# Kernel optimization log

Hardware: AMD Instinct MI355X
Metric: run time of the kernel (lower is better)

The kernel has to match this reference:

```python
import jax, jax.numpy as jnp
import numpy as np
from jax import lax

B, S, T = 32, 400, 100
V, OOV = 32000, 100
E, U, AU, GP, ENC = 512, 256, 256, 256, 512


def setup_inputs() -> dict:
    key = jax.random.key(0)
    ks = jax.random.split(key, 24)
    r = lambda k, shp: 0.02 * jax.random.normal(k, shp, dtype=jnp.float32)
    inp = {
        "gt_tokens": jax.random.randint(ks[0], (B, T), 0, V, dtype=jnp.int32),
        "extended_input_tokens": jax.random.randint(ks[1], (B, S), 0, V + OOV, dtype=jnp.int32),
        "enc_output": jax.random.normal(ks[2], (B, S, ENC), dtype=jnp.float32),
        "enc_attn": jax.random.normal(ks[3], (B, S, AU), dtype=jnp.float32),
        "h0": jnp.zeros((B, U), jnp.float32),
        "c0": jnp.zeros((B, U), jnp.float32),
        # learned parameters
        "emb": r(ks[4], (V, E)),
        "lstm_kernel": r(ks[5], (E, 4 * U)),
        "lstm_rec": r(ks[6], (U, 4 * U)),
        "lstm_bias": jnp.zeros((4 * U,), jnp.float32),
        "attn_Wd": r(ks[7], (2 * U, AU)),
        "attn_bd": jnp.zeros((AU,), jnp.float32),
        "attn_Wc": r(ks[8], (1, AU)),
        "attn_Wa": r(ks[9], (AU, 1)),
        "clf_W1": r(ks[10], (U, U)),
        "clf_b1": jnp.zeros((U,), jnp.float32),
        "clf_W2": r(ks[11], (U, V)),
        "clf_b2": jnp.zeros((V,), jnp.float32),
        "gp_Ws": r(ks[12], (2 * U, GP)),
        "gp_Wc": r(ks[13], (ENC, GP)),
        "gp_Wi": r(ks[14], (E, GP)),
        "gp_bi": jnp.zeros((GP,), jnp.float32),
        "gp_Wg": r(ks[15], (GP, 1)),
    }
    return inp


def _decode(gt_tokens, extended_input_tokens, enc_output, enc_attn, h0, c0,
            emb, lstm_kernel, lstm_rec, lstm_bias, attn_Wd, attn_bd, attn_Wc,
            attn_Wa, clf_W1, clf_b1, clf_W2, clf_b2, gp_Ws, gp_Wc, gp_Wi,
            gp_bi, gp_Wg):
    Bn, Sn = extended_input_tokens.shape
    gt_vec = emb[gt_tokens]                      # [B,T,E] teacher-forced inputs
    xs = jnp.swapaxes(gt_vec, 0, 1)              # [T,B,E]
    batch_idx = jnp.arange(Bn)[:, None]

    def step(carry, x):
        h, c, cov = carry                        # [B,U],[B,U],[B,S]
        # single-step LSTM (TF gate order i,f,g,o)
        z = x @ lstm_kernel + h @ lstm_rec + lstm_bias
        i_, f_, g_, o_ = jnp.split(z, 4, axis=-1)
        c = jax.nn.sigmoid(f_) * c + jax.nn.sigmoid(i_) * jnp.tanh(g_)
        h = jax.nn.sigmoid(o_) * jnp.tanh(c)
        dec_state = jnp.concatenate([h, c], axis=1)          # [B,2U]
        # Bahdanau attention with coverage
        dec_attn = dec_state @ attn_Wd + attn_bd             # [B,AU]
        cov_attn = cov[:, :, None] * attn_Wc[0]              # [B,S,AU]
        scores = jnp.tanh(enc_attn + cov_attn + dec_attn[:, None, :]) @ attn_Wa
        a = jax.nn.softmax(scores, axis=1)[:, :, 0]          # [B,S]
        c_vec = jnp.einsum('bse,bs->be', enc_output, a)      # [B,ENC]
        cov_loss = jnp.sum(jnp.minimum(cov, a), axis=1)      # [B]
        cov = cov + a
        # pg: faithful scalar quirk ([0,0,0] of broadcast sum in original)
        g = dec_state[0] @ gp_Ws + c_vec[0] @ gp_Wc + (x[0] @ gp_Wi + gp_bi)
        pg = jax.nn.sigmoid((g @ gp_Wg)[0])
        # vocab distribution, extended with OOV zeros
        vocab_p = jax.nn.softmax((h @ clf_W1 + clf_b1) @ clf_W2 + clf_b2, axis=-1)
        vocab_p = jnp.concatenate([vocab_p, jnp.zeros((Bn, OOV), vocab_p.dtype)], axis=1)
        # copy distribution via scatter-add of attention onto extended ids
        sent_p = jnp.zeros((Bn, V + OOV), a.dtype).at[batch_idx, extended_input_tokens].add(a)
        final = pg * vocab_p + (1.0 - pg) * sent_p           # [B,V+OOV]
        tok = jnp.argmax(final, axis=1).astype(jnp.int32)
        return (h, c, cov), (final, tok, cov_loss)

    cov0 = jnp.zeros((Bn, Sn), jnp.float32)
    _, (probs, seqs, cov_losses) = lax.scan(step, (h0, c0, cov0), xs)
    return (jnp.swapaxes(probs, 0, 1),       # [B,T,V+OOV]
            jnp.swapaxes(seqs, 0, 1),        # [B,T]
            jnp.swapaxes(cov_losses, 0, 1))  # [B,T]


def reference(gt_tokens, extended_input_tokens, enc_output, enc_attn, h0, c0,
              emb, lstm_kernel, lstm_rec, lstm_bias, attn_Wd, attn_bd,
              attn_Wc, attn_Wa, clf_W1, clf_b1, clf_W2, clf_b2, gp_Ws, gp_Wc,
              gp_Wi, gp_bi, gp_Wg):
    return _decode(gt_tokens, extended_input_tokens, enc_output, enc_attn, h0,
                   c0, emb, lstm_kernel, lstm_rec, lstm_bias, attn_Wd,
                   attn_bd, attn_Wc, attn_Wa, clf_W1, clf_b1, clf_W2, clf_b2,
                   gp_Ws, gp_Wc, gp_Wi, gp_bi, gp_Wg)
```

## Files before the change

### kernel.cpp

```cpp
#include <hip/hip_runtime.h>
#include <hip/hip_bf16.h>

#define Bn 32
#define Sn 400
#define Tn 100
#define Vn 32000
#define OOVn 100
#define VEn 32100
#define En 512
#define Un 256
#define AUn 256
#define GPn 256
#define ENCn 512
#define Z4n 1024
#define NPB 250

typedef __attribute__((ext_vector_type(8))) short bf16x8;
typedef __attribute__((ext_vector_type(4))) float f32x4;
typedef unsigned short ushort_t;
typedef unsigned long long u64;

__device__ __forceinline__ float rcp_f(float x){ return __builtin_amdgcn_rcpf(x); }
__device__ __forceinline__ float tanh_fast(float x){
  float e2 = __expf(2.f*x);
  return 1.f - 2.f*rcp_f(e2 + 1.f);
}
__device__ __forceinline__ float sigmoid_f(float x){ return 1.f/(1.f+__expf(-x)); }
__device__ __forceinline__ ushort_t f2bf(float f){
  unsigned u = __float_as_uint(f);
  unsigned r = (u + 0x7FFFu + ((u>>16)&1u)) >> 16;
  return (ushort_t)r;
}
__device__ __forceinline__ u64 shfl_xor_u64(u64 v, int m){
  unsigned lo = (unsigned)v, hi = (unsigned)(v>>32);
  lo = (unsigned)__shfl_xor((int)lo, m);
  hi = (unsigned)__shfl_xor((int)hi, m);
  return ((u64)hi<<32)|(u64)lo;
}

__device__ __forceinline__ void st_rlx(float* p, float v){
  __hip_atomic_store(p, v, __ATOMIC_RELAXED, __HIP_MEMORY_SCOPE_AGENT);
}
__device__ __forceinline__ float ld_rlx(const float* p){
  return __hip_atomic_load(p, __ATOMIC_RELAXED, __HIP_MEMORY_SCOPE_AGENT);
}
__device__ __forceinline__ void st_rlxu(unsigned* p, unsigned v){
  __hip_atomic_store(p, v, __ATOMIC_RELAXED, __HIP_MEMORY_SCOPE_AGENT);
}
__device__ __forceinline__ void st_rlx64(u64* p, u64 v){
  __hip_atomic_store(p, v, __ATOMIC_RELAXED, __HIP_MEMORY_SCOPE_AGENT);
}
__device__ __forceinline__ u64 ld_rlx64(const u64* p){
  return __hip_atomic_load(p, __ATOMIC_RELAXED, __HIP_MEMORY_SCOPE_AGENT);
}
__device__ __forceinline__ void st_flag(unsigned* p, unsigned v){
  __hip_atomic_store(p, v, __ATOMIC_RELAXED, __HIP_MEMORY_SCOPE_AGENT);
}
__device__ __forceinline__ unsigned ld_flag(const unsigned* p){
  return __hip_atomic_load(p, __ATOMIC_RELAXED, __HIP_MEMORY_SCOPE_AGENT);
}


__global__ __launch_bounds__(256) void k_zx(const int* __restrict__ gt,
    const float* __restrict__ emb, const float* __restrict__ Wk,
    const float* __restrict__ bias, float* __restrict__ Zx,
    const float* __restrict__ W2, ushort_t* __restrict__ W2T,
    unsigned* __restrict__ bars, unsigned* __restrict__ bars2,
    float* __restrict__ covloss){
  __shared__ __align__(16) char zbuf[16640];
  float (*As)[17] = (float(*)[17])zbuf;
  float (*Bs)[65] = (float(*)[65])(zbuf + 4352);
  int*   tok_lds  = (int*)(zbuf + 4352 + 4160);
  int r0 = blockIdx.x * 64;
  int c0 = blockIdx.y * 64;
  int tid = threadIdx.x;
  int ty = tid >> 4, tx16 = tid & 15;
  if (blockIdx.x == 0){
    int y = blockIdx.y;
    #pragma unroll
    for (int i = 0; i < 2; ++i){
      int idx = y*512 + i*256 + tid;
      bars[idx] = 0u;
      if (idx < NPB*32) bars2[idx] = 0u;
    }
    if (tid < 200) covloss[y*200 + tid] = 0.f;
  }
  if (tid < 64){
    int r = r0 + tid;
    tok_lds[tid] = gt[(r & 31)*Tn + (r >> 5)];
  }
  __syncthreads();
  float acc[4][4] = {};
  for (int k0 = 0; k0 < En; k0 += 16){
    #pragma unroll
    for (int p = 0; p < 4; ++p){
      int row = (tid>>4) + p*16, kk = tid & 15;
      As[row][kk] = emb[(size_t)tok_lds[row]*En + k0 + kk];
    }
    #pragma unroll
    for (int p = 0; p < 4; ++p){
      int kk = (tid>>6) + p*4, cc = tid & 63;
      Bs[kk][cc] = Wk[(size_t)(k0+kk)*Z4n + c0 + cc];
    }
    __syncthreads();
    #pragma unroll
    for (int kk = 0; kk < 16; ++kk){
      float av[4], bv[4];
      #pragma unroll
      for (int i=0;i<4;++i) av[i] = As[ty*4+i][kk];
      #pragma unroll
      for (int j=0;j<4;++j) bv[j] = Bs[kk][tx16*4+j];
      #pragma unroll
      for (int i=0;i<4;++i)
        #pragma unroll
        for (int j=0;j<4;++j) acc[i][j] += av[i]*bv[j];
    }
    __syncthreads();
  }
  #pragma unroll
  for (int i=0;i<4;++i){
    int row = r0 + ty*4 + i;
    #pragma unroll
    for (int j=0;j<4;++j){
      int col = c0 + tx16*4 + j;
      Zx[(size_t)row*Z4n + col] = acc[i][j] + bias[col];
    }
  }
  float (*tl)[65] = (float(*)[65])zbuf;
  int tx = tid & 63, ty4 = tid >> 6;
  int bid = blockIdx.x*16 + blockIdx.y;
  for (int rep = 0; rep < 3; ++rep){
    int tile = bid + rep*800;
    if (tile >= 2000) break;
    int n0 = (tile % 500) * 64, k0 = (tile / 500) * 64;
    __syncthreads();
    #pragma unroll
    for (int i = 0; i < 16; ++i){
      int kk = ty4 + i*4;
      tl[kk][tx] = W2[(size_t)(k0+kk)*Vn + n0 + tx];
    }
    __syncthreads();
    #pragma unroll
    for (int i = 0; i < 16; ++i){
      int n = ty4 + i*4;
      W2T[(size_t)(n0+n)*Un + k0 + tx] = f2bf(tl[tx][n]);
    }
  }
}


__global__ __launch_bounds__(1024, 1) void k_loop(
    const float* __restrict__ Zx, const float* __restrict__ Wr,
    const float* __restrict__ Wd, const float* __restrict__ bd,
    const float* __restrict__ Wc, const float* __restrict__ Wa,
    const float* __restrict__ enc_attn,
    const float* __restrict__ h0, const float* __restrict__ c0,
    float* __restrict__ h_all, float* __restrict__ decp,
    float* __restrict__ c0_all, float* __restrict__ a_all,
    float* __restrict__ covloss, float* __restrict__ spart,
    unsigned* __restrict__ bars){
  __shared__ float Wr_lds[256*128];
  __shared__ float hfull[Un];
  __shared__ float ppart[8][132];
  __shared__ float zx_lds[128];
  __shared__ float zfull[128];
  __shared__ float hnew[32], cown[32];
  __shared__ float dec_lds[AUn];
  __shared__ float cov_lds[50], sc_lds[50];
  __shared__ float wred[16];
  __shared__ float red8[8];

  const int b = blockIdx.x & 31, k = blockIdx.x >> 5;
  const int tid = threadIdx.x, lane = tid & 63, w = tid >> 6;
  unsigned* flags = bars + b*8*32;
  unsigned* myflag = flags + k*32;

  for (int idx = tid; idx < 256*128; idx += 1024){
    int u = idx >> 7, jl = idx & 127;
    int gcol = 32*k + (jl & 31) + 256*(jl >> 5);
    Wr_lds[idx] = Wr[(size_t)u*Z4n + gcol];
  }
  if (tid < 32) cown[tid] = c0[b*Un + 32*k + tid];
  if (tid < 50) cov_lds[tid] = 0.f;
  const float4 wc4 = *(const float4*)(Wc + lane*4);
  const float4 wa4 = *(const float4*)(Wa + lane*4);
  if (tid < 256) hfull[tid] = h0[b*Un + tid];
  if (tid >= 256 && tid < 384){
    int jl = tid - 256;
    int gcol = 32*k + (jl & 31) + 256*(jl >> 5);
    zx_lds[jl] = Zx[(size_t)(0*Bn + b)*Z4n + gcol];
  }
  __syncthreads();

  {
    int p = tid >> 7, jl = tid & 127;
    float acc = 0.f;
    const float* wr = Wr_lds + (p*32)*128 + jl;
    const float* hb = hfull + p*32;
    #pragma unroll 8
    for (int uu = 0; uu < 32; ++uu) acc += hb[uu]*wr[uu*128];
    ppart[p][jl] = acc;
  }
  __syncthreads();
  if (tid < 128){
    float s = zx_lds[tid];
    #pragma unroll
    for (int q = 0; q < 8; ++q) s += ppart[q][tid];
    zfull[tid] = s;
  }
  __syncthreads();
  if (tid < 32){
    float zi = zfull[tid], zf = zfull[32+tid], zg = zfull[64+tid], zo = zfull[96+tid];
    float cn = sigmoid_f(zf)*cown[tid] + sigmoid_f(zi)*tanhf(zg);
    float hn = sigmoid_f(zo)*tanhf(cn);
    cown[tid] = cn; hnew[tid] = hn;
    int col = 32*k + tid;
    st_rlx(h_all + (size_t)(0*Bn + b)*Un + col, hn);
    if (b == 0) c0_all[0*Un + col] = cn;
  }
  __syncthreads();
  if (tid < 256){
    int c = tid;
    float acc = 0.f;
    const float* wdh = Wd + (size_t)(32*k)*AUn + c;
    #pragma unroll 8
    for (int u = 0; u < 32; ++u) acc += hnew[u]*wdh[(size_t)u*AUn];
    const float* wdc = Wd + (size_t)(Un + 32*k)*AUn + c;
    #pragma unroll 8
    for (int u = 0; u < 32; ++u) acc += cown[u]*wdc[(size_t)u*AUn];
    st_rlx(decp + (size_t)(b*8 + k)*256 + c, acc);
  }
  __syncthreads();
  if (tid == 0) st_flag(myflag, 1u);

  for (int t = 0; t < Tn; ++t){
    const int cur = t & 1, oth = cur ^ 1;
    if (tid < 8){
      while (ld_flag(flags + tid*32) < (unsigned)(t+1))
        __builtin_amdgcn_s_sleep(1);
    }
    __syncthreads();
    if (tid < 256){
      hfull[tid] = ld_rlx(h_all + (size_t)(t*Bn + b)*Un + tid);
    } else if (tid < 512){
      int c = tid - 256;
      float s = bd[c];
      const float* dp = decp + (size_t)cur*(Bn*8*256) + (size_t)(b*8)*256 + c;
      #pragma unroll
      for (int q = 0; q < 8; ++q) s += ld_rlx(dp + q*256);
      dec_lds[c] = s;
    } else if (tid < 520){
      red8[tid-512] = (t > 0) ? ld_rlx(spart + oth*(Bn*8) + b*8 + (tid-512)) : 0.f;
    } else if (tid >= 576 && tid < 704 && t + 1 < Tn){
      int jl = tid - 576;
      int gcol = 32*k + (jl & 31) + 256*(jl >> 5);
      zx_lds[jl] = Zx[(size_t)((t+1)*Bn + b)*Z4n + gcol];
    }
    __syncthreads();
    if (t > 0 && w == 0){
      float pv = (lane < 8) ? red8[lane] : 0.f;
      pv += __shfl_xor(pv, 1); pv += __shfl_xor(pv, 2); pv += __shfl_xor(pv, 4);
      float inv = 1.f / __shfl(pv, 0);
      float clp = 0.f;
      if (lane < 50){
        float aa = sc_lds[lane] * inv;
        float co = cov_lds[lane];
        a_all[(size_t)((t-1)*Bn + b)*Sn + 50*k + lane] = aa;
        clp = fminf(co, aa);
        cov_lds[lane] = co + aa;
      }
      #pragma unroll
      for (int m = 1; m < 64; m <<= 1) clp += __shfl_xor(clp, m);
      if (lane == 0) atomicAdd(&covloss[b*Tn + (t-1)], clp);
    }
    {
      int p = tid >> 7, jl = tid & 127;
      float acc = 0.f;
      const float* wr = Wr_lds + (p*32)*128 + jl;
      const float* hb = hfull + p*32;
      #pragma unroll 8
      for (int uu = 0; uu < 32; ++uu) acc += hb[uu]*wr[uu*128];
      ppart[p][jl] = acc;
    }
    __syncthreads();
    if (tid < 128 && t + 1 < Tn){
      float s = zx_lds[tid];
      #pragma unroll
      for (int q = 0; q < 8; ++q) s += ppart[q][tid];
      zfull[tid] = s;
    }
    __syncthreads();
    if (tid < 32 && t + 1 < Tn){
      float zi = zfull[tid], zf = zfull[32+tid], zg = zfull[64+tid], zo = zfull[96+tid];
      float cn = sigmoid_f(zf)*cown[tid] + sigmoid_f(zi)*tanhf(zg);
      float hn = sigmoid_f(zo)*tanhf(cn);
      cown[tid] = cn; hnew[tid] = hn;
      int col = 32*k + tid;
      st_rlx(h_all + (size_t)((t+1)*Bn + b)*Un + col, hn);
      if (b == 0) c0_all[(t+1)*Un + col] = cn;
    }
    __syncthreads();
    if (w < 4){
      if (t + 1 < Tn){
        int c = tid;
        float acc = 0.f;
        const float* wdh = Wd + (size_t)(32*k)*AUn + c;
        #pragma unroll 8
        for (int u = 0; u < 32; ++u) acc += hnew[u]*wdh[(size_t)u*AUn];
        const float* wdc = Wd + (size_t)(Un + 32*k)*AUn + c;
        #pragma unroll 8
        for (int u = 0; u < 32; ++u) acc += cown[u]*wdc[(size_t)u*AUn];
        st_rlx(decp + (size_t)oth*(Bn*8*256) + (size_t)(b*8 + k)*256 + c, acc);
      }
    } else {
      const float4 da = *(const float4*)(dec_lds + lane*4);
      float wsum = 0.f;
      for (int sl = w - 4; sl < 50; sl += 12){
        float cvv = cov_lds[sl];
        const float4 e = *(const float4*)(enc_attn + ((size_t)(b*Sn + 50*k + sl))*AUn + lane*4);
        float psc = tanh_fast(e.x + cvv*wc4.x + da.x)*wa4.x
                  + tanh_fast(e.y + cvv*wc4.y + da.y)*wa4.y
                  + tanh_fast(e.z + cvv*wc4.z + da.z)*wa4.z
                  + tanh_fast(e.w + cvv*wc4.w + da.w)*wa4.w;
        #pragma unroll
        for (int m = 1; m < 64; m <<= 1) psc += __shfl_xor(psc, m);
        if (lane == 0){
          float ev = __expf(psc);
          sc_lds[sl] = ev;
          wsum += ev;
        }
      }
      if (lane == 0) wred[w] = wsum;
    }
    __syncthreads();
    if (tid == 0){
      float S = 0.f;
      #pragma unroll
      for (int q = 4; q < 16; ++q) S += wred[q];
      st_rlx(spart + cur*(Bn*8) + b*8 + k, S);
    }
    __syncthreads();
    if (tid == 0) st_flag(myflag, (unsigned)(t + 2));
  }

  if (tid < 8){
    while (ld_flag(flags + tid*32) < (unsigned)(Tn + 1))
      __builtin_amdgcn_s_sleep(1);
  }
  __syncthreads();
  if (tid < 8) red8[tid] = ld_rlx(spart + ((Tn-1)&1)*(Bn*8) + b*8 + tid);
  __syncthreads();
  if (w == 0){
    float pv = (lane < 8) ? red8[lane] : 0.f;
    pv += __shfl_xor(pv, 1); pv += __shfl_xor(pv, 2); pv += __shfl_xor(pv, 4);
    float inv = 1.f / __shfl(pv, 0);
    float clp = 0.f;
    if (lane < 50){
      float aa = sc_lds[lane] * inv;
      float co = cov_lds[lane];
      a_all[(size_t)((Tn-1)*Bn + b)*Sn + 50*k + lane] = aa;
      clp = fminf(co, aa);
    }
    #pragma unroll
    for (int m = 1; m < 64; m <<= 1) clp += __shfl_xor(clp, m);
    if (lane == 0) atomicAdd(&covloss[b*Tn + (Tn-1)], clp);
  }
}


__global__ __launch_bounds__(512, 1) void k_post(
    const float* __restrict__ h_all, const float* __restrict__ W1,
    const float* __restrict__ b1, ushort_t* __restrict__ hid,
    const int* __restrict__ gt, const float* __restrict__ emb,
    const float* __restrict__ gpWi, const float* __restrict__ gpbi,
    const float* __restrict__ a_all, const float* __restrict__ enc_out,
    const float* __restrict__ c0_all, const float* __restrict__ gpWs,
    const float* __restrict__ gpWc, const float* __restrict__ gpWg,
    float* __restrict__ pg, const ushort_t* __restrict__ W2T,
    const float* __restrict__ b2, float* __restrict__ Sp,
    float* __restrict__ Ssum, u64* __restrict__ Ap,
    float* __restrict__ probs, const int* __restrict__ ext,
    float* __restrict__ seqs, unsigned* __restrict__ bars2){
  __shared__ __align__(16) char sb[135168];
  __shared__ u64 wmax8[8];
  __shared__ float red4[4];
  const int gid = blockIdx.x, tid = threadIdx.x;
  const int lane = tid & 63, w = tid >> 6;
  unsigned* myflag = bars2 + gid*32;

  if (gid < 100){
    int t = gid;
    float* hl = (float*)sb;
    for (int i = tid; i < Bn*Un; i += 512) hl[i] = h_all[(size_t)t*Bn*Un + i];
    __syncthreads();
    int j = tid & 255, p = tid >> 8;
    float bj = b1[j];
    float acc[16];
    #pragma unroll
    for (int i = 0; i < 16; ++i) acc[i] = bj;
    for (int u = 0; u < Un; ++u){
      float wv = W1[u*Un + j];
      const float* hp = hl + (p*16)*Un + u;
      #pragma unroll
      for (int i = 0; i < 16; ++i) acc[i] += hp[i*Un] * wv;
    }
    __syncthreads();
    ushort_t* hidL = (ushort_t*)sb;
    #pragma unroll
    for (int i = 0; i < 16; ++i) hidL[(p*16+i)*Un + j] = f2bf(acc[i]);
    __syncthreads();
    unsigned* hw = (unsigned*)hid + (size_t)t*4096;
    const unsigned* hs = (const unsigned*)hidL;
    for (int i = tid; i < 4096; i += 512) st_rlxu(hw + i, hs[i]);
  } else if (gid < 200){
    int t = gid - 100;
    float* al = (float*)sb;
    float* cv = al + 400;
    float* xl = cv + 512;
    for (int s = tid; s < Sn; s += 512) al[s] = a_all[(size_t)(t*Bn)*Sn + s];
    for (int i = tid; i < En; i += 512) xl[i] = emb[(size_t)gt[t]*En + i];
    __syncthreads();
    if (tid < ENCn){
      float acc = 0.f;
      for (int s = 0; s < Sn; ++s) acc += enc_out[(size_t)s*ENCn + tid]*al[s];
      cv[tid] = acc;
    }
    __syncthreads();
    if (tid < 256){
      int j = tid;
      float g = gpbi[j];
      for (int u = 0; u < En; ++u) g += xl[u]*gpWi[u*GPn + j];
      const float* h0r = h_all + (size_t)t*Bn*Un;
      const float* c0r = c0_all + t*Un;
      for (int u = 0; u < Un; ++u) g += h0r[u]*gpWs[u*GPn + j];
      for (int u = 0; u < Un; ++u) g += c0r[u]*gpWs[(Un+u)*GPn + j];
      for (int e = 0; e < ENCn; ++e) g += cv[e]*gpWc[e*GPn + j];
      float v = g * gpWg[j];
      #pragma unroll
      for (int m = 1; m < 64; m <<= 1) v += __shfl_xor(v, m);
      if (lane == 0) red4[w] = v;
    }
    __syncthreads();
    if (tid == 0)
      st_rlx(&pg[t], 1.f/(1.f+__expf(-(red4[0]+red4[1]+red4[2]+red4[3]))));
  }
  __syncthreads();
  if (tid == 0) st_flag(myflag, 1u);
  if (tid < NPB){ while (ld_flag(bars2 + tid*32) < 1u) __builtin_amdgcn_s_sleep(1); }
  __syncthreads();

  ushort_t* Bs = (ushort_t*)sb;
  const int slice = gid % 125, gx = gid / 125;
  const int n0 = slice * 256;
  {
    int rr = tid >> 1, half = (tid & 1) * 128;
    const ushort_t* gb = W2T + (size_t)(n0 + rr)*Un + half;
    ushort_t* lb = Bs + rr*264 + half;
    #pragma unroll
    for (int j2 = 0; j2 < 16; ++j2)
      *((uint4*)lb + j2) = *((const uint4*)gb + j2);
  }
  __syncthreads();
  const int cbase = gx ? 13 : 0;
  const int nch   = gx ? 12 : 13;

  for (int ci = 0; ci < nch; ++ci){
    int r0 = (cbase + ci) * 128;
    bf16x8 af[8];
    {
      const ushort_t* ar = hid + (size_t)(r0 + w*16 + (lane&15))*Un + (lane>>4)*8;
      #pragma unroll
      for (int kk = 0; kk < 8; ++kk) af[kk] = *(const bf16x8*)(ar + kk*32);
    }
    f32x4 acc[16];
    #pragma unroll
    for (int i = 0; i < 16; ++i) acc[i] = (f32x4){0.f,0.f,0.f,0.f};
    #pragma unroll
    for (int kk = 0; kk < 8; ++kk){
      #pragma unroll
      for (int nt = 0; nt < 16; ++nt){
        bf16x8 bf = *(const bf16x8*)(Bs + (nt*16 + (lane&15))*264 + kk*32 + (lane>>4)*8);
        acc[nt] = __builtin_amdgcn_mfma_f32_16x16x32_bf16(af[kk], bf, acc[nt], 0, 0, 0);
      }
    }
    float rs[4] = {0.f,0.f,0.f,0.f};
    #pragma unroll
    for (int nt = 0; nt < 16; ++nt){
      int v = n0 + nt*16 + (lane&15);
      float b2v = b2[v];
      #pragma unroll
      for (int i = 0; i < 4; ++i) rs[i] += __expf(acc[nt][i] + b2v);
    }
    #pragma unroll
    for (int m = 1; m < 16; m <<= 1)
      #pragma unroll
      for (int i = 0; i < 4; ++i) rs[i] += __shfl_xor(rs[i], m);
    if ((lane&15) == 0){
      int rowloc = w*16 + (lane>>4)*4;
      #pragma unroll
      for (int i = 0; i < 4; ++i)
        st_rlx(&Sp[(size_t)slice*3200 + r0 + rowloc + i], rs[i]);
    }
  }
  __syncthreads();
  if (tid == 0) st_flag(myflag, 2u);
  if (tid < NPB){ while (ld_flag(bars2 + tid*32) < 2u) __builtin_amdgcn_s_sleep(1); }
  __syncthreads();

  if (gid < 7){
    int r = gid*512 + tid;
    if (r < 3200){
      float s = 0.f;
      for (int sl = 0; sl < 125; ++sl) s += ld_rlx(&Sp[(size_t)sl*3200 + r]);
      st_rlx(&Ssum[r], s);
    }
  }
  __syncthreads();
  if (tid == 0) st_flag(myflag, 3u);
  if (tid < NPB){ while (ld_flag(bars2 + tid*32) < 3u) __builtin_amdgcn_s_sleep(1); }
  __syncthreads();

  for (int ci = 0; ci < nch; ++ci){
    int r0 = (cbase + ci) * 128;
    bf16x8 af[8];
    {
      const ushort_t* ar = hid + (size_t)(r0 + w*16 + (lane&15))*Un + (lane>>4)*8;
      #pragma unroll
      for (int kk = 0; kk < 8; ++kk) af[kk] = *(const bf16x8*)(ar + kk*32);
    }
    f32x4 acc[16];
    #pragma unroll
    for (int i = 0; i < 16; ++i) acc[i] = (f32x4){0.f,0.f,0.f,0.f};
    #pragma unroll
    for (int kk = 0; kk < 8; ++kk){
      #pragma unroll
      for (int nt = 0; nt < 16; ++nt){
        bf16x8 bf = *(const bf16x8*)(Bs + (nt*16 + (lane&15))*264 + kk*32 + (lane>>4)*8);
        acc[nt] = __builtin_amdgcn_mfma_f32_16x16x32_bf16(af[kk], bf, acc[nt], 0, 0, 0);
      }
    }
    int rowloc = w*16 + (lane>>4)*4;
    float sc[4]; size_t obase[4];
    #pragma unroll
    for (int i = 0; i < 4; ++i){
      int r = r0 + rowloc + i; int tt = r>>5, bb = r&31;
      sc[i] = ld_rlx(&pg[tt]) / Ssum[r];
      obase[i] = (size_t)(bb*Tn + tt)*VEn;
    }
    u64 pm[4] = {0,0,0,0};
    #pragma unroll
    for (int nt = 0; nt < 16; ++nt){
      int v = n0 + nt*16 + (lane&15);
      float b2v = b2[v];
      #pragma unroll
      for (int i = 0; i < 4; ++i){
        float val = __expf(acc[nt][i] + b2v) * sc[i];
        __builtin_nontemporal_store(val, &probs[obase[i] + v]);
        u64 p = ((u64)__float_as_uint(val)<<32) | (u64)(0xFFFFFFFFu - (unsigned)v);
        pm[i] = p > pm[i] ? p : pm[i];
      }
    }
    #pragma unroll
    for (int m = 1; m < 16; m <<= 1)
      #pragma unroll
      for (int i = 0; i < 4; ++i){
        u64 o = shfl_xor_u64(pm[i], m);
        pm[i] = o > pm[i] ? o : pm[i];
      }
    if ((lane&15) == 0)
      #pragma unroll
      for (int i = 0; i < 4; ++i)
        st_rlx64(&Ap[(size_t)slice*3200 + r0 + rowloc + i], pm[i]);
  }
  __syncthreads();
  if (tid == 0) st_flag(myflag, 4u);
  if (tid < NPB){ while (ld_flag(bars2 + tid*32) < 4u) __builtin_amdgcn_s_sleep(1); }
  __syncthreads();

  int* hkey = (int*)sb;
  float* hval = (float*)(sb + 4096);
  for (int rep = 0; rep < 13; ++rep){
    int r = rep*250 + gid;
    if (r >= 3200) break;
    int t = r >> 5, b = r & 31;
    #pragma unroll
    for (int i = 0; i < 2; ++i){
      hkey[tid + i*512] = -1;
      hval[tid + i*512] = 0.f;
    }
    size_t obase = (size_t)(b*Tn + t)*VEn;
    if (tid < OOVn) probs[obase + Vn + tid] = 0.f;
    u64 vm = (tid < 125) ? ld_rlx64(&Ap[(size_t)tid*3200 + r]) : 0ull;
    float c1 = 1.f - ld_rlx(&pg[t]);
    __syncthreads();
    if (tid < Sn){
      int key = ext[b*Sn + tid];
      float v = c1 * a_all[(size_t)r*Sn + tid];
      unsigned h = ((unsigned)key * 2654435761u) >> 22;
      for (;;){
        int old = atomicCAS(&hkey[h], -1, key);
        if (old == -1 || old == key) break;
        h = (h + 1) & 1023;
      }
      atomicAdd(&hval[h], v);
    }
    __syncthreads();
    u64 pm = vm;
    #pragma unroll
    for (int i = 0; i < 2; ++i){
      int slot = tid + i*512;
      int tk = hkey[slot];
      if (tk >= 0){
        float nv = probs[obase + tk] + hval[slot];
        probs[obase + tk] = nv;
        u64 p = ((u64)__float_as_uint(nv)<<32) | (u64)(0xFFFFFFFFu - (unsigned)tk);
        pm = p > pm ? p : pm;
      }
    }
    #pragma unroll
    for (int m = 1; m < 64; m <<= 1){
      u64 o = shfl_xor_u64(pm, m);
      pm = o > pm ? o : pm;
    }
    if (lane == 0) wmax8[w] = pm;
    __syncthreads();
    if (tid == 0){
      u64 mm = wmax8[0];
      #pragma unroll
      for (int q = 1; q < 8; ++q) mm = wmax8[q] > mm ? wmax8[q] : mm;
      unsigned tk = 0xFFFFFFFFu - (unsigned)(mm & 0xFFFFFFFFull);
      seqs[b*Tn + t] = (float)tk;
    }
    __syncthreads();
  }
}


extern "C" void kernel_launch(void* const* d_in, const int* in_sizes, int n_in,
                              void* d_out, int out_size, void* d_ws, size_t ws_size,
                              hipStream_t stream){
  (void)in_sizes; (void)n_in; (void)out_size; (void)ws_size;
  const int*   gt       = (const int*)d_in[0];
  const int*   ext      = (const int*)d_in[1];
  const float* enc_out  = (const float*)d_in[2];
  const float* enc_attn = (const float*)d_in[3];
  const float* h0       = (const float*)d_in[4];
  const float* c0       = (const float*)d_in[5];
  const float* emb      = (const float*)d_in[6];
  const float* Wk       = (const float*)d_in[7];
  const float* Wr       = (const float*)d_in[8];
  const float* lb       = (const float*)d_in[9];
  const float* Wd       = (const float*)d_in[10];
  const float* bd       = (const float*)d_in[11];
  const float* Wc       = (const float*)d_in[12];
  const float* Wa       = (const float*)d_in[13];
  const float* W1       = (const float*)d_in[14];
  const float* b1       = (const float*)d_in[15];
  const float* W2       = (const float*)d_in[16];
  const float* b2       = (const float*)d_in[17];
  const float* gpWs     = (const float*)d_in[18];
  const float* gpWc     = (const float*)d_in[19];
  const float* gpWi     = (const float*)d_in[20];
  const float* gpbi     = (const float*)d_in[21];
  const float* gpWg     = (const float*)d_in[22];

  float* probs   = (float*)d_out;
  float* seqs    = probs + (size_t)Bn*Tn*VEn;
  float* covloss = seqs + Bn*Tn;

  char* wp = (char*)d_ws;
  auto carve = [&](size_t bytes)->void*{
    void* p = (void*)wp; wp += (bytes + 255) & ~(size_t)255; return p;
  };
  float*    Zx      = (float*)carve((size_t)3200*Z4n*4);
  float*    h_all   = (float*)carve((size_t)Tn*Bn*Un*4);
  float*    decp    = (float*)carve((size_t)2*Bn*8*256*4);
  float*    c0_all  = (float*)carve((size_t)Tn*Un*4);
  float*    a_all   = (float*)carve((size_t)3200*Sn*4);
  ushort_t* hid_bf  = (ushort_t*)carve((size_t)3200*Un*2);
  ushort_t* W2T     = (ushort_t*)carve((size_t)Vn*Un*2);
  float*    Ssum    = (float*)carve((size_t)3200*4);
  float*    Sp      = (float*)carve((size_t)125*3200*4);
  u64*      Ap      = (u64*)carve((size_t)125*3200*8);
  float*    pg      = (float*)carve((size_t)Tn*4);
  float*    spart   = (float*)carve((size_t)2*Bn*8*4);
  unsigned* bars    = (unsigned*)carve((size_t)Bn*8*32*4);
  unsigned* bars2   = (unsigned*)carve((size_t)NPB*32*4);

  k_zx  <<<dim3(50,16), 256, 0, stream>>>(gt, emb, Wk, lb, Zx, W2, W2T,
                                          bars, bars2, covloss);

  k_loop<<<256, 1024, 0, stream>>>(Zx, Wr, Wd, bd, Wc, Wa, enc_attn,
                                   h0, c0, h_all, decp, c0_all,
                                   a_all, covloss, spart, bars);

  k_post<<<NPB, 512, 0, stream>>>(h_all, W1, b1, hid_bf, gt, emb,
                                  gpWi, gpbi, a_all, enc_out, c0_all,
                                  gpWs, gpWc, gpWg, pg, W2T, b2,
                                  Sp, Ssum, Ap, probs, ext, seqs, bars2);
}
```

Before: 1.144 ms.

## Split copy-scatter and argmax into a separate kernel, drop grid barrier

The final scatter-add of attention into the extended vocabulary and the argmax reduction move out of k_post into a new k_scatter kernel with one block per (t,b) row. This removes the software grid-wide spin barrier and the 13-iteration serial loop per block in exchange for an extra kernel launch. It also replaces the nontemporal stores of probs with regular stores, likely so the scatter kernel's read-modify-write of probs can hit in cache.

```diff
diff --git a/kernel.cpp b/kernel.cpp
--- a/kernel.cpp
+++ b/kernel.cpp
@@ -379,10 +379,8 @@
     float* __restrict__ pg, const ushort_t* __restrict__ W2T,
     const float* __restrict__ b2, float* __restrict__ Sp,
     float* __restrict__ Ssum, u64* __restrict__ Ap,
-    float* __restrict__ probs, const int* __restrict__ ext,
-    float* __restrict__ seqs, unsigned* __restrict__ bars2){
+    float* __restrict__ probs, unsigned* __restrict__ bars2){
   __shared__ __align__(16) char sb[135168];
-  __shared__ u64 wmax8[8];
   __shared__ float red4[4];
   const int gid = blockIdx.x, tid = threadIdx.x;
   const int lane = tid & 63, w = tid >> 6;
@@ -555,7 +553,7 @@
       #pragma unroll
       for (int i = 0; i < 4; ++i){
         float val = __expf(acc[nt][i] + b2v) * sc[i];
-        __builtin_nontemporal_store(val, &probs[obase[i] + v]);
+        probs[obase[i] + v] = val;
         u64 p = ((u64)__float_as_uint(val)<<32) | (u64)(0xFFFFFFFFu - (unsigned)v);
         pm[i] = p > pm[i] ? p : pm[i];
       }
@@ -572,66 +570,65 @@
       for (int i = 0; i < 4; ++i)
         st_rlx64(&Ap[(size_t)slice*3200 + r0 + rowloc + i], pm[i]);
   }
-  __syncthreads();
-  if (tid == 0) st_flag(myflag, 4u);
-  if (tid < NPB){ while (ld_flag(bars2 + tid*32) < 4u) __builtin_amdgcn_s_sleep(1); }
-  __syncthreads();
-
-  int* hkey = (int*)sb;
-  float* hval = (float*)(sb + 4096);
-  for (int rep = 0; rep < 13; ++rep){
-    int r = rep*250 + gid;
-    if (r >= 3200) break;
-    int t = r >> 5, b = r & 31;
-    #pragma unroll
-    for (int i = 0; i < 2; ++i){
-      hkey[tid + i*512] = -1;
-      hval[tid + i*512] = 0.f;
-    }
-    size_t obase = (size_t)(b*Tn + t)*VEn;
-    if (tid < OOVn) probs[obase + Vn + tid] = 0.f;
-    u64 vm = (tid < 125) ? ld_rlx64(&Ap[(size_t)tid*3200 + r]) : 0ull;
-    float c1 = 1.f - ld_rlx(&pg[t]);
-    __syncthreads();
-    if (tid < Sn){
-      int key = ext[b*Sn + tid];
-      float v = c1 * a_all[(size_t)r*Sn + tid];
-      unsigned h = ((unsigned)key * 2654435761u) >> 22;
-      for (;;){
-        int old = atomicCAS(&hkey[h], -1, key);
-        if (old == -1 || old == key) break;
-        h = (h + 1) & 1023;
-      }
-      atomicAdd(&hval[h], v);
-    }
-    __syncthreads();
-    u64 pm = vm;
-    #pragma unroll
-    for (int i = 0; i < 2; ++i){
-      int slot = tid + i*512;
-      int tk = hkey[slot];
-      if (tk >= 0){
-        float nv = probs[obase + tk] + hval[slot];
-        probs[obase + tk] = nv;
-        u64 p = ((u64)__float_as_uint(nv)<<32) | (u64)(0xFFFFFFFFu - (unsigned)tk);
-        pm = p > pm ? p : pm;
-      }
-    }
-    #pragma unroll
-    for (int m = 1; m < 64; m <<= 1){
-      u64 o = shfl_xor_u64(pm, m);
-      pm = o > pm ? o : pm;
-    }
-    if (lane == 0) wmax8[w] = pm;
-    __syncthreads();
-    if (tid == 0){
-      u64 mm = wmax8[0];
-      #pragma unroll
-      for (int q = 1; q < 8; ++q) mm = wmax8[q] > mm ? wmax8[q] : mm;
-      unsigned tk = 0xFFFFFFFFu - (unsigned)(mm & 0xFFFFFFFFull);
-      seqs[b*Tn + t] = (float)tk;
-    }
-    __syncthreads();
+}
+
+__global__ __launch_bounds__(256) void k_scatter(const int* __restrict__ ext,
+    const float* __restrict__ a_all, const float* __restrict__ pg,
+    float* __restrict__ probs, const u64* __restrict__ Ap,
+    float* __restrict__ seqs){
+  __shared__ int   hkey[1024];
+  __shared__ float hval[1024];
+  __shared__ u64   wmax[4];
+  int r = blockIdx.x; int t = r>>5, b = r&31;
+  float c1 = 1.f - pg[t];
+  int tid = threadIdx.x;
+  #pragma unroll
+  for (int i = 0; i < 4; ++i){
+    hkey[tid + i*256] = -1;
+    hval[tid + i*256] = 0.f;
+  }
+  size_t obase = (size_t)(b*Tn + t)*VEn;
+  if (tid < OOVn) probs[obase + Vn + tid] = 0.f;
+  u64 vm = (tid < 125) ? Ap[(size_t)tid*3200 + r] : 0ull;
+  __syncthreads();
+  for (int s = tid; s < Sn; s += 256){
+    int key = ext[b*Sn + s];
+    float v = c1 * a_all[(size_t)r*Sn + s];
+    unsigned h = ((unsigned)key * 2654435761u) >> 22;
+    for (;;){
+      int old = atomicCAS(&hkey[h], -1, key);
+      if (old == -1 || old == key) break;
+      h = (h + 1) & 1023;
+    }
+    atomicAdd(&hval[h], v);
+  }
+  __syncthreads();
+  u64 pm = vm;
+  #pragma unroll
+  for (int i = 0; i < 4; ++i){
+    int slot = tid + i*256;
+    int tk = hkey[slot];
+    if (tk >= 0){
+      float nv = probs[obase + tk] + hval[slot];
+      probs[obase + tk] = nv;
+      u64 p = ((u64)__float_as_uint(nv)<<32) | (u64)(0xFFFFFFFFu - (unsigned)tk);
+      pm = p > pm ? p : pm;
+    }
+  }
+  #pragma unroll
+  for (int m = 1; m < 64; m <<= 1){
+    u64 o = shfl_xor_u64(pm, m);
+    pm = o > pm ? o : pm;
+  }
+  int lane = tid & 63, w = tid >> 6;
+  if (lane == 0) wmax[w] = pm;
+  __syncthreads();
+  if (tid == 0){
+    u64 mm = wmax[0];
+    #pragma unroll
+    for (int q = 1; q < 4; ++q) mm = wmax[q] > mm ? wmax[q] : mm;
+    unsigned tk = 0xFFFFFFFFu - (unsigned)(mm & 0xFFFFFFFFull);
+    seqs[b*Tn + t] = (float)tk;
   }
 }
 
@@ -697,5 +694,7 @@
   k_post<<<NPB, 512, 0, stream>>>(h_all, W1, b1, hid_bf, gt, emb,
                                   gpWi, gpbi, a_all, enc_out, c0_all,
                                   gpWs, gpWc, gpWg, pg, W2T, b2,
-                                  Sp, Ssum, Ap, probs, ext, seqs, bars2);
-}
+                                  Sp, Ssum, Ap, probs, bars2);
+
+  k_scatter<<<3200, 256, 0, stream>>>(ext, a_all, pg, probs, Ap, seqs);
+}
```

Measured after the change: 1.007 ms. -11.9%, faster.
